# Kernel optimization log

Hardware: AMD Instinct MI355X
Metric: run time of the kernel (lower is better)

The kernel has to match this reference:

```python
import jax, jax.numpy as jnp
import numpy as np

EPS = 1e-6
N_HEAD, N_KV_HEAD = 16, 4
VE_GATE_CH = 12

def rmsnorm(x):
    return x * jax.lax.rsqrt(jnp.mean(x * x, axis=-1, keepdims=True) + EPS)

def apply_rotary_emb(x, cos, sin):
    half = x.shape[-1] // 2
    x1, x2 = x[..., :half], x[..., half:]
    return jnp.concatenate([x1 * cos + x2 * sin, -x1 * sin + x2 * cos], axis=-1)

def setup_inputs():
    key = jax.random.key(0)
    ks = jax.random.split(key, 8)
    B, S, D = 2, 2048, 1024
    H, KVH = N_HEAD, N_KV_HEAD
    hd = D // H
    x = jax.random.normal(ks[0], (B, S, D), jnp.float32)
    ve = jax.random.normal(ks[1], (B, S, KVH * hd), jnp.float32)
    # real rotary tables, broadcastable over [B,S,H,hd//2]
    inv_freq = 1.0 / (10000.0 ** (np.arange(hd // 2, dtype=np.float32) / (hd // 2)))
    ang = np.arange(S, dtype=np.float32)[:, None] * inv_freq[None, :]  # [S, hd//2]
    cos = jnp.asarray(np.cos(ang))[:, None, :]  # [S,1,hd//2]
    sin = jnp.asarray(np.sin(ang))[:, None, :]
    std = 0.02
    Wq = jax.random.normal(ks[2], (D, H * hd), jnp.float32) * std
    Wk = jax.random.normal(ks[3], (D, KVH * hd), jnp.float32) * std
    Wv = jax.random.normal(ks[4], (D, KVH * hd), jnp.float32) * std
    Wo = jax.random.normal(ks[5], (D, D), jnp.float32) * std
    Wg = jax.random.normal(ks[6], (VE_GATE_CH, KVH), jnp.float32) * std
    return {"x": x, "ve": ve, "cos": cos, "sin": sin, "Wq": Wq, "Wk": Wk,
            "Wv": Wv, "Wo": Wo, "Wg": Wg, "window_size": 512}

def reference(x, ve, cos, sin, Wq, Wk, Wv, Wo, Wg, window_size):
    B, S, D = x.shape
    H, KVH = N_HEAD, N_KV_HEAD
    hd = D // H
    q = (x @ Wq).reshape(B, S, H, hd)
    k = (x @ Wk).reshape(B, S, KVH, hd)
    v = (x @ Wv).reshape(B, S, KVH, hd)
    # value-embedding gating
    gate = 3.0 * jax.nn.sigmoid(x[..., :VE_GATE_CH] @ Wg)  # [B,S,KVH]
    v = v + gate[..., None] * ve.reshape(B, S, KVH, hd)
    # RoPE + QK rmsnorm * 1.2
    q = rmsnorm(apply_rotary_emb(q, cos, sin)) * 1.2
    k = rmsnorm(apply_rotary_emb(k, cos, sin)) * 1.2
    # GQA head repeat (repeat_interleave over head dim)
    rep = H // KVH
    k = jnp.repeat(k, rep, axis=2)  # [B,S,H,hd]
    v = jnp.repeat(v, rep, axis=2)
    scale = 1.0 / np.sqrt(hd).astype(np.float32)
    scores = jnp.einsum('bqhd,bkhd->bhqk', q, k) * scale  # [B,H,S,S]
    pos = jnp.arange(S)
    allow = (pos[None, :] <= pos[:, None]) & (pos[None, :] >= pos[:, None] - window_size + 1)
    scores = jnp.where(allow[None, None], scores, -jnp.inf)
    attn = jax.nn.softmax(scores, axis=-1)
    y = jnp.einsum('bhqk,bkhd->bqhd', attn, v).reshape(B, S, D)
    return y @ Wo
```

## Files before the change

kernel.cpp:

```cpp
#include <hip/hip_runtime.h>
#include <hip/hip_bf16.h>
#include <cstddef>
#include <cstdint>


typedef short v8s __attribute__((ext_vector_type(8)));
typedef float v4f __attribute__((ext_vector_type(4)));

__device__ __forceinline__ ushort b1(float a) {
  uint u = __float_as_uint(a);
  return (ushort)((u + 0x7FFFu + ((u >> 16) & 1u)) >> 16);
}
__device__ __forceinline__ uint bpack(float lo, float hi) {
  uint ul = __float_as_uint(lo), uh = __float_as_uint(hi);
  ul = (ul + 0x7FFFu + ((ul >> 16) & 1u)) >> 16;
  uh = (uh + 0x7FFFu + ((uh >> 16) & 1u)) & 0xFFFF0000u;
  return ul | uh;
}

__device__ __forceinline__ void async16(const ushort* g, ushort* l) {
  __builtin_amdgcn_global_load_lds(
      (__attribute__((address_space(1))) void*)(uintptr_t)(const void*)g,
      (__attribute__((address_space(3))) void*)(uintptr_t)(void*)l, 16, 0, 0);
}

__global__ __launch_bounds__(256) void prep_all(
    const float* __restrict__ x, ushort* __restrict__ xb,
    const float* __restrict__ Wg, float* __restrict__ gates,
    const float* __restrict__ cosp, const float* __restrict__ sinp,
    float2* __restrict__ cs,
    const float* __restrict__ Wq, const float* __restrict__ Wk,
    const float* __restrict__ Wv, const float* __restrict__ Wo,
    ushort* __restrict__ Wqt, ushort* __restrict__ Wkt,
    ushort* __restrict__ Wvt, ushort* __restrict__ Wot)
{
  const int bx = blockIdx.x, t = threadIdx.x;
  if (bx < 4096) {
    const float* row = x + (size_t)bx * 1024;
    float4 v = *(const float4*)(row + t * 4);
    ushort4 o;
    o.x = b1(v.x); o.y = b1(v.y); o.z = b1(v.z); o.w = b1(v.w);
    *(ushort4*)(xb + (size_t)bx * 1024 + t * 4) = o;
    if (t < 4) {
      float g = 0.f;
#pragma unroll
      for (int i = 0; i < 12; ++i) g += row[i] * Wg[i * 4 + t];
      gates[bx * 4 + t] = 3.0f / (1.0f + __expf(-g));
    }
    return;
  }
  if (bx < 4352) {
    const int i = (bx - 4096) * 256 + t;
    cs[i] = make_float2(cosp[i], sinp[i]);
    return;
  }
  __shared__ ushort tile[32][33];
  int u = bx - 4352;
  const float* W; ushort* Wt; int N, xx, yy;
  if (u < 1024)      { W = Wq; Wt = Wqt; N = 1024; xx = u & 31; yy = u >> 5; }
  else if (u < 2048) { u -= 1024; W = Wo; Wt = Wot; N = 1024; xx = u & 31; yy = u >> 5; }
  else if (u < 2304) { u -= 2048; W = Wk; Wt = Wkt; N = 256;  xx = u & 7;  yy = u >> 3; }
  else               { u -= 2304; W = Wv; Wt = Wvt; N = 256;  xx = u & 7;  yy = u >> 3; }
  const int n0 = xx * 32, k0 = yy * 32;
  const int tx = t & 31, ty = t >> 5;
#pragma unroll
  for (int i = 0; i < 4; ++i) {
    const int k = ty + i * 8;
    tile[k][tx] = b1(W[(size_t)(k0 + k) * N + n0 + tx]);
  }
  __syncthreads();
#pragma unroll
  for (int i = 0; i < 4; ++i) {
    const int n = ty + i * 8;
    Wt[(size_t)(n0 + n) * 1024 + k0 + tx] = tile[tx][n];
  }
}

__device__ __forceinline__ void gemm_mainloop(
    const ushort* __restrict__ A, const ushort* __restrict__ Bt,
    int K, int m0, int n0, ushort (*As)[64], ushort (*Bs)[64],
    v4f acc[2][4])
{
  const int t = threadIdx.x;
  const int lane = t & 63, wave = t >> 6;
  const int wr = wave >> 1, wc = wave & 1;
  const int quad = lane >> 4, l16 = lane & 15;
  const int l8 = lane >> 3;
  const int c8s = ((lane & 7) ^ l8) * 8;
  const int sc = (l16 & 7) * 8;

  const ushort* ap[2];
  ushort* al[2];
#pragma unroll
  for (int i = 0; i < 2; ++i) {
    const int row = wave * 8 + i * 32 + l8;
    ap[i] = A + (size_t)(m0 + row) * K + c8s;
    al[i] = &As[wave * 8 + i * 32][0];
  }
  const ushort* bp[4];
  ushort* bl[4];
#pragma unroll
  for (int i = 0; i < 4; ++i) {
    const int row = (wave * 4 + i) * 8 + l8;
    bp[i] = Bt + (size_t)(n0 + row) * K + c8s;
    bl[i] = &Bs[(wave * 4 + i) * 8][0];
  }

  auto stage = [&](int buf, int k0) {
#pragma unroll
    for (int i = 0; i < 2; ++i) async16(ap[i] + k0, al[i] + buf * (64 * 64));
#pragma unroll
    for (int i = 0; i < 4; ++i) async16(bp[i] + k0, bl[i] + buf * (128 * 64));
  };
  auto compute = [&](int buf) {
#pragma unroll
    for (int ks = 0; ks < 2; ++ks) {
      const int col = (ks * 32 + quad * 8) ^ sc;
      v8s af[2], bf[4];
#pragma unroll
      for (int i = 0; i < 2; ++i)
        af[i] = *(const v8s*)&As[buf * 64 + wr * 32 + i * 16 + l16][col];
#pragma unroll
      for (int i = 0; i < 4; ++i)
        bf[i] = *(const v8s*)&Bs[buf * 128 + wc * 64 + i * 16 + l16][col];
#pragma unroll
      for (int mt = 0; mt < 2; ++mt)
#pragma unroll
        for (int nt = 0; nt < 4; ++nt)
          acc[mt][nt] = __builtin_amdgcn_mfma_f32_16x16x32_bf16(
              af[mt], bf[nt], acc[mt][nt], 0, 0, 0);
    }
  };

  stage(0, 0);
  __syncthreads();
  int buf = 0;
  for (int k0 = 64; k0 < K; k0 += 64) {
    stage(buf ^ 1, k0);
    compute(buf);
    __syncthreads();
    buf ^= 1;
  }
  compute(buf);
}

__device__ __forceinline__ void gemm_mainloop32(
    const ushort* __restrict__ A, const ushort* __restrict__ Bt,
    int K, int m0, int n0, ushort (*As)[64], ushort (*Bs)[64],
    v4f acc[4])
{
  const int t = threadIdx.x;
  const int lane = t & 63, wave = t >> 6;
  const int wr = wave >> 1, wc = wave & 1;
  const int quad = lane >> 4, l16 = lane & 15;
  const int l8 = lane >> 3;
  const int c8s = ((lane & 7) ^ l8) * 8;
  const int sc = (l16 & 7) * 8;

  const ushort* ap = A + (size_t)(m0 + wave * 8 + l8) * K + c8s;
  ushort* al = &As[wave * 8][0];
  const ushort* bp[4];
  ushort* bl[4];
#pragma unroll
  for (int i = 0; i < 4; ++i) {
    const int row = (wave * 4 + i) * 8 + l8;
    bp[i] = Bt + (size_t)(n0 + row) * K + c8s;
    bl[i] = &Bs[(wave * 4 + i) * 8][0];
  }

  auto stage = [&](int buf, int k0) {
    async16(ap + k0, al + buf * (32 * 64));
#pragma unroll
    for (int i = 0; i < 4; ++i) async16(bp[i] + k0, bl[i] + buf * (128 * 64));
  };
  auto compute = [&](int buf) {
#pragma unroll
    for (int ks = 0; ks < 2; ++ks) {
      const int col = (ks * 32 + quad * 8) ^ sc;
      v8s af = *(const v8s*)&As[buf * 32 + wr * 16 + l16][col];
      v8s bf[4];
#pragma unroll
      for (int i = 0; i < 4; ++i)
        bf[i] = *(const v8s*)&Bs[buf * 128 + wc * 64 + i * 16 + l16][col];
#pragma unroll
      for (int nt = 0; nt < 4; ++nt)
        acc[nt] = __builtin_amdgcn_mfma_f32_16x16x32_bf16(af, bf[nt], acc[nt], 0, 0, 0);
    }
  };

  stage(0, 0);
  __syncthreads();
  int buf = 0;
  for (int k0 = 64; k0 < K; k0 += 64) {
    stage(buf ^ 1, k0);
    compute(buf);
    __syncthreads();
    buf ^= 1;
  }
  compute(buf);
}

__global__ __launch_bounds__(256) void gemm_qkv_fused(
    const ushort* __restrict__ A, const ushort* __restrict__ Bt,
    const float2* __restrict__ cs, const float* __restrict__ gates,
    const float* __restrict__ ve,
    ushort* __restrict__ qb, ushort* __restrict__ kb, ushort* __restrict__ vb)
{
  __shared__ ushort As[128][64];
  __shared__ ushort Bs[256][64];
  const int lin = blockIdx.y * 64 + blockIdx.x;
  const int swz = (lin & 7) * 96 + (lin >> 3);
  const int x8 = swz / 96, local = swz % 96;
  const int bxx = x8 * 8 + (local & 7), sec = local >> 3;
  const int m0 = bxx * 64, n0 = sec * 128;
  const int lane = threadIdx.x & 63, wave = threadIdx.x >> 6;
  const int wr = wave >> 1, wc = wave & 1;
  const int quad = lane >> 4, l16 = lane & 15;

  v4f acc[2][4];
#pragma unroll
  for (int i = 0; i < 2; ++i)
#pragma unroll
    for (int j = 0; j < 4; ++j) acc[i][j] = (v4f){0.f, 0.f, 0.f, 0.f};

  gemm_mainloop(A, Bt, 1024, m0, n0, As, Bs, acc);

  const int head_col = n0 + wc * 64;

  if (sec < 10) {
    const bool isQ = (sec < 8);
    const int h = (head_col - (isQ ? 0 : 1024)) >> 6;
    ushort* dst = isQ ? qb : kb;
    const int ld = isQ ? 1024 : 256;
#pragma unroll
    for (int mt = 0; mt < 2; ++mt)
#pragma unroll
      for (int r = 0; r < 4; ++r) {
        const int row = m0 + wr * 32 + mt * 16 + quad * 4 + r;
        const int s = row & 2047;
        const float2 cs0 = cs[s * 32 + l16];
        const float2 cs1 = cs[s * 32 + 16 + l16];
        const float x10 = acc[mt][0][r], x11 = acc[mt][1][r];
        const float x20 = acc[mt][2][r], x21 = acc[mt][3][r];
        float ss = x10 * x10 + x11 * x11 + x20 * x20 + x21 * x21;
        ss += __shfl_xor(ss, 1);
        ss += __shfl_xor(ss, 2);
        ss += __shfl_xor(ss, 4);
        ss += __shfl_xor(ss, 8);
        const float rs = rsqrtf(ss * (1.0f / 64.0f) + 1e-6f) * 1.2f;
        ushort* dp = dst + (size_t)row * ld + h * 64 + l16;
        dp[0]  = b1((x10 * cs0.x + x20 * cs0.y) * rs);
        dp[16] = b1((x11 * cs1.x + x21 * cs1.y) * rs);
        dp[32] = b1((-x10 * cs0.y + x20 * cs0.x) * rs);
        dp[48] = b1((-x11 * cs1.y + x21 * cs1.x) * rs);
      }
  } else {
    const int kvh = (head_col - 1280) >> 6;
#pragma unroll
    for (int mt = 0; mt < 2; ++mt)
#pragma unroll
      for (int r = 0; r < 4; ++r) {
        const int row = m0 + wr * 32 + mt * 16 + quad * 4 + r;
        const float gate = gates[row * 4 + kvh];
        const float* vep = ve + (size_t)row * 256 + kvh * 64 + l16;
        ushort* dp = vb + (size_t)row * 256 + kvh * 64 + l16;
#pragma unroll
        for (int nt = 0; nt < 4; ++nt)
          dp[nt * 16] = b1(acc[mt][nt][r] + gate * vep[nt * 16]);
      }
  }
}

__global__ __launch_bounds__(256) void gemm_wo(
    const ushort* __restrict__ A, const ushort* __restrict__ Bt,
    float* __restrict__ C)
{
  __shared__ ushort As[64][64];
  __shared__ ushort Bs[256][64];
  const int lin = blockIdx.y * 128 + blockIdx.x;
  const int swz = (lin & 7) * 128 + (lin >> 3);
  const int x8 = swz >> 7, local = swz & 127;
  const int bxx = x8 * 16 + (local & 15), byy = local >> 4;
  const int m0 = bxx * 32, n0 = byy * 128;
  const int lane = threadIdx.x & 63, wave = threadIdx.x >> 6;
  const int wr = wave >> 1, wc = wave & 1;
  const int quad = lane >> 4, l16 = lane & 15;

  v4f acc[4];
#pragma unroll
  for (int j = 0; j < 4; ++j) acc[j] = (v4f){0.f, 0.f, 0.f, 0.f};

  gemm_mainloop32(A, Bt, 1024, m0, n0, As, Bs, acc);

#pragma unroll
  for (int r = 0; r < 4; ++r) {
    float* cp = C + (size_t)(m0 + wr * 16 + quad * 4 + r) * 1024
                  + n0 + wc * 64 + l16;
#pragma unroll
    for (int nt = 0; nt < 4; ++nt) cp[nt * 16] = acc[nt][r];
  }
}

__global__ __launch_bounds__(256) void transpose_v(
    const ushort* __restrict__ vb, ushort* __restrict__ vtb)
{
  __shared__ ushort L[64][72];
  const int s0 = blockIdx.x * 64, kvh = blockIdx.y, b = blockIdx.z;
  const int t = threadIdx.x;
#pragma unroll
  for (int i = 0; i < 2; ++i) {
    const int cc = t + i * 256;
    const int srow = cc >> 3, c8 = (cc & 7) * 8;
    *(int4*)&L[srow][c8] =
        *(const int4*)(vb + ((size_t)(b * 2048 + s0 + srow)) * 256 + kvh * 64 + c8);
  }
  __syncthreads();
#pragma unroll
  for (int i = 0; i < 2; ++i) {
    const int cc = t + i * 256;
    const int drow = cc >> 3, s8 = (cc & 7) * 8;
    ushort w[8];
#pragma unroll
    for (int jj = 0; jj < 8; ++jj) w[jj] = L[s8 + jj][drow];
    *(int4*)(vtb + ((size_t)((b * 4 + kvh) * 64 + drow)) * 2048 + s0 + s8) =
        *(int4*)w;
  }
}

__global__ __launch_bounds__(256) void attn_mfma(
    const ushort* __restrict__ qb, const ushort* __restrict__ kb,
    const ushort* __restrict__ vtb, ushort* __restrict__ yb,
    const int* __restrict__ wptr)
{
  __shared__ ushort Ks[64][72];
  __shared__ ushort Vt[80][72];
  __shared__ ushort Ps[64][72];
  const int lin = (blockIdx.z * 16 + blockIdx.y) * 32 + blockIdx.x;
  const int swz = (lin & 7) * 128 + (lin >> 3);
  const int x8 = swz >> 7, local = swz & 127;
  const int qt = local & 31;
  const int hb = x8 * 4 + (local >> 5);
  const int h = hb & 15, b = hb >> 4;
  const int kvh = h >> 2, q0 = qt * 64;
  const int t = threadIdx.x, lane = t & 63, wave = t >> 6;
  const int quad = lane >> 4, l16 = lane & 15;
  const int Wwin = *wptr;

  v8s qf0, qf1;
  {
    const ushort* qp = qb + ((size_t)(b * 2048 + q0 + wave * 16 + l16)) * 1024
                          + h * 64 + quad * 8;
    qf0 = *(const v8s*)qp;
    qf1 = *(const v8s*)(qp + 32);
  }

  if (t < 128) {
    const int row = 64 + (t >> 3), c8 = (t & 7) * 8;
    const int v = (row == 64) ? 0x3F803F80 : 0;
    int4 w; w.x = v; w.y = v; w.z = v; w.w = v;
    *(int4*)&Vt[row][c8] = w;
  }

  v4f o[5];
#pragma unroll
  for (int d = 0; d < 5; ++d) o[d] = (v4f){0.f, 0.f, 0.f, 0.f};

  const int lo = q0 - Wwin + 1;
  const int kt0 = (lo > 0) ? (lo >> 6) : 0;
  const int kt1 = (q0 + 63) >> 6;

  for (int kt = kt0; kt <= kt1; ++kt) {
#pragma unroll
    for (int i = 0; i < 2; ++i) {
      const int cc = t + i * 256;
      const int r8 = cc >> 3, c8 = (cc & 7) * 8;
      *(int4*)&Ks[r8][c8] =
          *(const int4*)(kb + ((size_t)(b * 2048 + kt * 64 + r8)) * 256 + kvh * 64 + c8);
      *(int4*)&Vt[r8][c8] =
          *(const int4*)(vtb + ((size_t)((b * 4 + kvh) * 64 + r8)) * 2048 + kt * 64 + c8);
    }
    __syncthreads();

    const bool needs_mask = (kt * 64 + 63 > q0) || (kt * 64 < q0 + 64 - Wwin);

    {
      const int qrow = q0 + wave * 16 + l16;
      ushort* prow = &Ps[wave * 16 + l16][0];
#pragma unroll
      for (int nt = 0; nt < 4; ++nt) {
        v8s kf0 = *(const v8s*)&Ks[nt * 16 + l16][quad * 8];
        v8s kf1 = *(const v8s*)&Ks[nt * 16 + l16][32 + quad * 8];
        v4f st = (v4f){0.f, 0.f, 0.f, 0.f};
        st = __builtin_amdgcn_mfma_f32_16x16x32_bf16(kf0, qf0, st, 0, 0, 0);
        st = __builtin_amdgcn_mfma_f32_16x16x32_bf16(kf1, qf1, st, 0, 0, 0);
        float p[4];
#pragma unroll
        for (int r = 0; r < 4; ++r) {
          p[r] = exp2f(fmaf(st[r], 0.18033688011f, -17.31234049107f));
          if (needs_mask) {
            const int k = kt * 64 + nt * 16 + quad * 4 + r;
            const bool ok = (k <= qrow) && (k > qrow - Wwin);
            p[r] = ok ? p[r] : 0.0f;
          }
        }
        uint2 w;
        w.x = bpack(p[0], p[1]);
        w.y = bpack(p[2], p[3]);
        *(uint2*)(prow + nt * 16 + quad * 4) = w;
      }
    }

    v8s pf0 = *(const v8s*)&Ps[wave * 16 + l16][quad * 8];
    v8s pf1 = *(const v8s*)&Ps[wave * 16 + l16][32 + quad * 8];
#pragma unroll
    for (int dt = 0; dt < 5; ++dt) {
      v8s vf0 = *(const v8s*)&Vt[dt * 16 + l16][quad * 8];
      v8s vf1 = *(const v8s*)&Vt[dt * 16 + l16][32 + quad * 8];
      o[dt] = __builtin_amdgcn_mfma_f32_16x16x32_bf16(pf0, vf0, o[dt], 0, 0, 0);
      o[dt] = __builtin_amdgcn_mfma_f32_16x16x32_bf16(pf1, vf1, o[dt], 0, 0, 0);
    }
    __syncthreads();
  }

#pragma unroll
  for (int r = 0; r < 4; ++r) {
    const float l = __shfl(o[4][r], lane & 48);
    const float inv = 1.0f / l;
    ushort* yp = yb + ((size_t)(b * 2048 + q0 + wave * 16 + quad * 4 + r)) * 1024
                    + h * 64 + l16;
#pragma unroll
    for (int dt = 0; dt < 4; ++dt) yp[dt * 16] = b1(o[dt][r] * inv);
  }
}

extern "C" void kernel_launch(void* const* d_in, const int* in_sizes, int n_in,
                              void* d_out, int out_size, void* d_ws, size_t ws_size,
                              hipStream_t stream)
{
  const float* x    = (const float*)d_in[0];
  const float* ve   = (const float*)d_in[1];
  const float* cosp = (const float*)d_in[2];
  const float* sinp = (const float*)d_in[3];
  const float* Wq   = (const float*)d_in[4];
  const float* Wk   = (const float*)d_in[5];
  const float* Wv   = (const float*)d_in[6];
  const float* Wo   = (const float*)d_in[7];
  const float* Wg   = (const float*)d_in[8];
  const int*   win  = (const int*)d_in[9];
  float* out = (float*)d_out;

  char* p = (char*)d_ws;
  ushort* xb    = (ushort*)p;  p += (size_t)4194304 * 2;
  ushort* qb    = (ushort*)p;  p += (size_t)4194304 * 2;
  ushort* yb    = (ushort*)p;  p += (size_t)4194304 * 2;
  ushort* kb    = (ushort*)p;  p += (size_t)1048576 * 2;
  ushort* vb    = (ushort*)p;  p += (size_t)1048576 * 2;
  ushort* vtb   = (ushort*)p;  p += (size_t)1048576 * 2;
  ushort* Wqkvt = (ushort*)p;  p += (size_t)1536 * 1024 * 2;
  ushort* Wot   = (ushort*)p;  p += (size_t)1048576 * 2;
  float2* cs    = (float2*)p;  p += (size_t)65536 * 8;
  float*  gates = (float*)p;

  prep_all<<<6912, 256, 0, stream>>>(
      x, xb, Wg, gates, cosp, sinp, cs, Wq, Wk, Wv, Wo,
      Wqkvt, Wqkvt + (size_t)1024 * 1024, Wqkvt + (size_t)1280 * 1024, Wot);

  gemm_qkv_fused<<<dim3(64, 12), 256, 0, stream>>>(xb, Wqkvt, cs, gates, ve,
                                                   qb, kb, vb);
  transpose_v<<<dim3(32, 4, 2), 256, 0, stream>>>(vb, vtb);

  attn_mfma<<<dim3(32, 16, 2), 256, 0, stream>>>(qb, kb, vtb, yb, win);

  gemm_wo<<<dim3(128, 8), 256, 0, stream>>>(yb, Wot, out);
}
```

Measured before the change: 155.5 us.

## Load K/V MFMA fragments directly from global memory, drop LDS staging and barriers

The attention kernel no longer stages K and V^T tiles in shared memory. Each lane loads its MFMA operand fragments straight from global memory, and both __syncthreads per key tile are removed. The row-sum column that was padded into the V tile is replaced by a register vector of bf16 ones fed to an extra MFMA. This cuts LDS traffic and block-wide synchronisation. In exchange, each wave issues redundant global loads of the same K/V data and global load latency is no longer hidden behind a shared staging step.

```diff
diff --git a/kernel.cpp b/kernel.cpp
--- a/kernel.cpp
+++ b/kernel.cpp
@@ -332,8 +332,6 @@
     const ushort* __restrict__ vtb, ushort* __restrict__ yb,
     const int* __restrict__ wptr)
 {
-  __shared__ ushort Ks[64][72];
-  __shared__ ushort Vt[80][72];
   __shared__ ushort Ps[64][72];
   const int lin = (blockIdx.z * 16 + blockIdx.y) * 32 + blockIdx.x;
   const int swz = (lin & 7) * 128 + (lin >> 3);
@@ -354,12 +352,9 @@
     qf1 = *(const v8s*)(qp + 32);
   }
 
-  if (t < 128) {
-    const int row = 64 + (t >> 3), c8 = (t & 7) * 8;
-    const int v = (row == 64) ? 0x3F803F80 : 0;
-    int4 w; w.x = v; w.y = v; w.z = v; w.w = v;
-    *(int4*)&Vt[row][c8] = w;
-  }
+  v8s vones;
+#pragma unroll
+  for (int i = 0; i < 8; ++i) vones[i] = (short)0x3F80;
 
   v4f o[5];
 #pragma unroll
@@ -369,57 +364,50 @@
   const int kt0 = (lo > 0) ? (lo >> 6) : 0;
   const int kt1 = (q0 + 63) >> 6;
 
+  const ushort* kfb = kb + ((size_t)(b * 2048 + l16)) * 256 + kvh * 64 + quad * 8;
+  const ushort* vfb = vtb + ((size_t)((b * 4 + kvh) * 64 + l16)) * 2048 + quad * 8;
+  const int qrow = q0 + wave * 16 + l16;
+  ushort* prow = &Ps[wave * 16 + l16][0];
+
   for (int kt = kt0; kt <= kt1; ++kt) {
-#pragma unroll
-    for (int i = 0; i < 2; ++i) {
-      const int cc = t + i * 256;
-      const int r8 = cc >> 3, c8 = (cc & 7) * 8;
-      *(int4*)&Ks[r8][c8] =
-          *(const int4*)(kb + ((size_t)(b * 2048 + kt * 64 + r8)) * 256 + kvh * 64 + c8);
-      *(int4*)&Vt[r8][c8] =
-          *(const int4*)(vtb + ((size_t)((b * 4 + kvh) * 64 + r8)) * 2048 + kt * 64 + c8);
-    }
-    __syncthreads();
-
     const bool needs_mask = (kt * 64 + 63 > q0) || (kt * 64 < q0 + 64 - Wwin);
 
-    {
-      const int qrow = q0 + wave * 16 + l16;
-      ushort* prow = &Ps[wave * 16 + l16][0];
-#pragma unroll
-      for (int nt = 0; nt < 4; ++nt) {
-        v8s kf0 = *(const v8s*)&Ks[nt * 16 + l16][quad * 8];
-        v8s kf1 = *(const v8s*)&Ks[nt * 16 + l16][32 + quad * 8];
-        v4f st = (v4f){0.f, 0.f, 0.f, 0.f};
-        st = __builtin_amdgcn_mfma_f32_16x16x32_bf16(kf0, qf0, st, 0, 0, 0);
-        st = __builtin_amdgcn_mfma_f32_16x16x32_bf16(kf1, qf1, st, 0, 0, 0);
-        float p[4];
-#pragma unroll
-        for (int r = 0; r < 4; ++r) {
-          p[r] = exp2f(fmaf(st[r], 0.18033688011f, -17.31234049107f));
-          if (needs_mask) {
-            const int k = kt * 64 + nt * 16 + quad * 4 + r;
-            const bool ok = (k <= qrow) && (k > qrow - Wwin);
-            p[r] = ok ? p[r] : 0.0f;
-          }
+#pragma unroll
+    for (int nt = 0; nt < 4; ++nt) {
+      const ushort* kp = kfb + (size_t)(kt * 64 + nt * 16) * 256;
+      v8s kf0 = *(const v8s*)kp;
+      v8s kf1 = *(const v8s*)(kp + 32);
+      v4f st = (v4f){0.f, 0.f, 0.f, 0.f};
+      st = __builtin_amdgcn_mfma_f32_16x16x32_bf16(kf0, qf0, st, 0, 0, 0);
+      st = __builtin_amdgcn_mfma_f32_16x16x32_bf16(kf1, qf1, st, 0, 0, 0);
+      float p[4];
+#pragma unroll
+      for (int r = 0; r < 4; ++r) {
+        p[r] = exp2f(fmaf(st[r], 0.18033688011f, -17.31234049107f));
+        if (needs_mask) {
+          const int k = kt * 64 + nt * 16 + quad * 4 + r;
+          const bool ok = (k <= qrow) && (k > qrow - Wwin);
+          p[r] = ok ? p[r] : 0.0f;
         }
-        uint2 w;
-        w.x = bpack(p[0], p[1]);
-        w.y = bpack(p[2], p[3]);
-        *(uint2*)(prow + nt * 16 + quad * 4) = w;
       }
+      uint2 w;
+      w.x = bpack(p[0], p[1]);
+      w.y = bpack(p[2], p[3]);
+      *(uint2*)(prow + nt * 16 + quad * 4) = w;
     }
 
     v8s pf0 = *(const v8s*)&Ps[wave * 16 + l16][quad * 8];
     v8s pf1 = *(const v8s*)&Ps[wave * 16 + l16][32 + quad * 8];
 #pragma unroll
-    for (int dt = 0; dt < 5; ++dt) {
-      v8s vf0 = *(const v8s*)&Vt[dt * 16 + l16][quad * 8];
-      v8s vf1 = *(const v8s*)&Vt[dt * 16 + l16][32 + quad * 8];
+    for (int dt = 0; dt < 4; ++dt) {
+      const ushort* vp = vfb + (size_t)(dt * 16) * 2048 + kt * 64;
+      v8s vf0 = *(const v8s*)vp;
+      v8s vf1 = *(const v8s*)(vp + 32);
       o[dt] = __builtin_amdgcn_mfma_f32_16x16x32_bf16(pf0, vf0, o[dt], 0, 0, 0);
       o[dt] = __builtin_amdgcn_mfma_f32_16x16x32_bf16(pf1, vf1, o[dt], 0, 0, 0);
     }
-    __syncthreads();
+    o[4] = __builtin_amdgcn_mfma_f32_16x16x32_bf16(pf0, vones, o[4], 0, 0, 0);
+    o[4] = __builtin_amdgcn_mfma_f32_16x16x32_bf16(pf1, vones, o[4], 0, 0, 0);
   }
 
 #pragma unroll
```

New measurement: 196.1 us. 26.1% more time.
